# Optimization experiments

Hardware: AMD Instinct MI355X
Metric: run time of the kernel (lower is better)

Reference implementation:

```python
import jax, jax.numpy as jnp
import numpy as np

N, C, H, W, D = 4, 320, 16, 16, 16
POS_RATIO = 0.5


def setup_inputs() -> dict:
    key = jax.random.key(0)
    k1, k2, k3, k4 = jax.random.split(key, 4)
    q = jax.random.normal(k1, (N, C, H, W, D), jnp.float32)
    k = jax.random.normal(k2, (N, C, H, W, D), jnp.float32)

    def make_coord(kr):
        # crop boxes: upper-left corner in [0, 0.4), extent in [0.4, 0.6)
        start = jax.random.uniform(kr, (N, 3), jnp.float32) * 0.4
        size = 0.4 + jax.random.uniform(jax.random.fold_in(kr, 1), (N, 3), jnp.float32) * 0.2
        return jnp.concatenate([start, start + size], axis=1)  # (N, 6)

    coord_q = make_coord(k3)
    coord_k = make_coord(k4)
    return {"q": q, "k": k, "coord_q": coord_q, "coord_k": coord_k}


def _centers(coord, h, w, d):
    """coord: (N,6) -> centers (N, h*w*d, 3) of each voxel in global coords, and bin diag (N,)."""
    dims = jnp.array([h, w, d], jnp.float32)
    bin_sz = (coord[:, 3:6] - coord[:, 0:3]) / dims  # (N,3) = (bin_h, bin_w, bin_d)
    ax = jnp.arange(h, dtype=jnp.float32) + 0.5
    ay = jnp.arange(w, dtype=jnp.float32) + 0.5
    az = jnp.arange(d, dtype=jnp.float32) + 0.5
    grid = jnp.stack(jnp.meshgrid(ax, ay, az, indexing="ij"), axis=-1)  # (h,w,d,3)
    grid = grid.reshape(1, h * w * d, 3)
    centers = grid * bin_sz[:, None, :] + coord[:, None, 0:3]  # (N, L, 3)
    diag = jnp.sqrt(jnp.sum(bin_sz ** 2, axis=-1))  # (N,)
    return centers, diag


def reference(q, k, coord_q, coord_k):
    n, c, h, w, d = q.shape
    L = h * w * d
    qf = q.reshape(n, c, L)
    kf = k.reshape(n, c, L)

    cq, diag_q = _centers(coord_q, h, w, d)  # (N,L,3), (N,)
    ck, diag_k = _centers(coord_k, h, w, d)
    max_diag = jnp.maximum(diag_q, diag_k)[:, None, None]  # (N,1,1)

    def masked_loss(q_flat, centers_q):
        # pairwise center distance (N, L, L) -- sum of three squared diffs, no (N,L,L,3) stack
        d2 = ((centers_q[:, :, None, 0] - ck[:, None, :, 0]) ** 2
              + (centers_q[:, :, None, 1] - ck[:, None, :, 1]) ** 2
              + (centers_q[:, :, None, 2] - ck[:, None, :, 2]) ** 2)
        dist = jnp.sqrt(d2) / max_diag
        mask = jax.lax.stop_gradient((dist < POS_RATIO).astype(jnp.float32))
        logit = jnp.einsum("ncl,ncm->nlm", q_flat, kf)  # bmm(q^T, k)
        return jnp.sum(logit * mask, axis=(-2, -1)) / (jnp.sum(mask, axis=(-2, -1)) + 1e-6)

    loss = masked_loss(qf, cq)
    # anatomy branch: flip(q) and flipped q-centers along batch dim 0 (as in source flip(x, dim=0))
    loss_rev = masked_loss(jnp.flip(qf, axis=0), jnp.flip(cq, axis=0))
    return -2.0 * jnp.mean(loss) - 2.0 * jnp.mean(loss_rev)
```

## Files before the change

kernel.cpp:

```cpp
#include <hip/hip_runtime.h>

#define LVOX   4096
#define NCH    320
#define NCOMBO 8
#define PCAP   65536

struct Geo {
    float qs0, qs1, qs2, qo0, qo1, qo2;
    float ks0, ks1, ks2, ko0, ko1, ko2;
    float ik0, ik1, ik2;
    float T;
};

__device__ __forceinline__ Geo make_geo(const float* __restrict__ cq,
                                        const float* __restrict__ ck,
                                        int n, int qb) {
    Geo g;
    const float* qc = cq + qb * 6;
    const float* qn = cq + n * 6;
    const float* kc = ck + n * 6;
    g.qs0 = (qc[3] - qc[0]) * (1.f / 16.f); g.qo0 = qc[0];
    g.qs1 = (qc[4] - qc[1]) * (1.f / 16.f); g.qo1 = qc[1];
    g.qs2 = (qc[5] - qc[2]) * (1.f / 16.f); g.qo2 = qc[2];
    g.ks0 = (kc[3] - kc[0]) * (1.f / 16.f); g.ko0 = kc[0];
    g.ks1 = (kc[4] - kc[1]) * (1.f / 16.f); g.ko1 = kc[1];
    g.ks2 = (kc[5] - kc[2]) * (1.f / 16.f); g.ko2 = kc[2];
    g.ik0 = 1.f / g.ks0; g.ik1 = 1.f / g.ks1; g.ik2 = 1.f / g.ks2;
    float b0 = (qn[3] - qn[0]) * (1.f / 16.f);
    float b1 = (qn[4] - qn[1]) * (1.f / 16.f);
    float b2 = (qn[5] - qn[2]) * (1.f / 16.f);
    float dq = sqrtf(b0 * b0 + b1 * b1 + b2 * b2);
    float dk = sqrtf(g.ks0 * g.ks0 + g.ks1 * g.ks1 + g.ks2 * g.ks2);
    g.T = 0.5f * fmaxf(dq, dk);
    return g;
}

__device__ __forceinline__ void axrange(float c, float ko, float ik, float T,
                                        int& m0, int& m1) {
    float lo = (c - T - ko) * ik - 0.5f;
    float hi = (c + T - ko) * ik - 0.5f;
    m0 = max((int)ceilf(lo) - 1, 0);
    m1 = min((int)floorf(hi) + 1, 15);
}

__global__ void enum_pairs(const float* __restrict__ coord_q,
                           const float* __restrict__ coord_k,
                           unsigned* __restrict__ pcnt,
                           unsigned* __restrict__ pairs, int cap) {
    int gid = blockIdx.x * 256 + threadIdx.x;
    int j = gid >> 12;
    int l = gid & 4095;
    int n = j & 3;
    int qb = (j & 4) ? (3 - n) : n;
    Geo g = make_geo(coord_q, coord_k, n, qb);

    int ix = l >> 8, iy = (l >> 4) & 15, iz = l & 15;
    float cx = (ix + 0.5f) * g.qs0 + g.qo0;
    float cy = (iy + 0.5f) * g.qs1 + g.qo1;
    float cz = (iz + 0.5f) * g.qs2 + g.qo2;
    int x0, x1, y0, y1, z0, z1;
    axrange(cx, g.ko0, g.ik0, g.T, x0, x1);
    axrange(cy, g.ko1, g.ik1, g.T, y0, y1);
    axrange(cz, g.ko2, g.ik2, g.T, z0, z1);

    int nh = 0;
    for (int x = x0; x <= x1; ++x) {
        float dx = cx - ((x + 0.5f) * g.ks0 + g.ko0);
        float dx2 = dx * dx;
        for (int y = y0; y <= y1; ++y) {
            float dy = cy - ((y + 0.5f) * g.ks1 + g.ko1);
            float dxy = dx2 + dy * dy;
            for (int z = z0; z <= z1; ++z) {
                float dz = cz - ((z + 0.5f) * g.ks2 + g.ko2);
                if (sqrtf(dxy + dz * dz) < g.T) nh++;
            }
        }
    }

    int lane = threadIdx.x & 63;
    int incl = nh;
#pragma unroll
    for (int off = 1; off < 64; off <<= 1) {
        int t = __shfl_up(incl, off, 64);
        if (lane >= off) incl += t;
    }
    int total = __shfl(incl, 63, 64);
    int base = 0;
    if (lane == 63) base = (int)atomicAdd(&pcnt[j], (unsigned)total);
    base = __shfl(base, 63, 64);
    int w = base + incl - nh;

    unsigned* out = pairs + (size_t)j * (size_t)cap;
    for (int x = x0; x <= x1; ++x) {
        float dx = cx - ((x + 0.5f) * g.ks0 + g.ko0);
        float dx2 = dx * dx;
        for (int y = y0; y <= y1; ++y) {
            float dy = cy - ((y + 0.5f) * g.ks1 + g.ko1);
            float dxy = dx2 + dy * dy;
            for (int z = z0; z <= z1; ++z) {
                float dz = cz - ((z + 0.5f) * g.ks2 + g.ko2);
                if (sqrtf(dxy + dz * dz) < g.T) {
                    if (w < cap)
                        out[w] = ((unsigned)l << 12) | (unsigned)((x << 8) | (y << 4) | z);
                    w++;
                }
            }
        }
    }
}

__global__ void __launch_bounds__(256) gather_lds(
        const float* __restrict__ q, const float* __restrict__ k,
        const unsigned* __restrict__ pcnt, const unsigned* __restrict__ pairs,
        int cap, float* __restrict__ S) {
    __shared__ float qrow[LVOX];
    __shared__ float krow[LVOX];
    __shared__ float sp[4];
    int j = blockIdx.x;
    int c = blockIdx.y;
    int n = j & 3;
    int qb = (j & 4) ? (3 - n) : n;
    const float* qsrc = q + ((size_t)(qb * NCH + c)) * LVOX;
    const float* ksrc = k + ((size_t)(n * NCH + c)) * LVOX;
    int t = threadIdx.x;

#pragma unroll
    for (int i = 0; i < 4; ++i) {
        int off = (t + 256 * i) * 4;
        *(float4*)&qrow[off] = *(const float4*)&qsrc[off];
        *(float4*)&krow[off] = *(const float4*)&ksrc[off];
    }
    __syncthreads();

    unsigned cnt = pcnt[j];
    if (cnt > (unsigned)cap) cnt = (unsigned)cap;
    const unsigned* pl = pairs + (size_t)j * (size_t)cap;

    float acc = 0.f;
    for (unsigned p = (unsigned)t; p < cnt; p += 256u) {
        unsigned pr = pl[p];
        acc += qrow[pr >> 12] * krow[pr & 4095u];
    }

#pragma unroll
    for (int off = 32; off; off >>= 1) acc += __shfl_down(acc, off, 64);
    int lane = t & 63;
    if (lane == 0) sp[t >> 6] = acc;
    __syncthreads();
    if (t == 0) atomicAdd(&S[j], sp[0] + sp[1] + sp[2] + sp[3]);
}

__global__ void finalize(const float* __restrict__ S,
                         const unsigned* __restrict__ pcnt,
                         float* __restrict__ out) {
    if (threadIdx.x == 0) {
        float t = 0.f;
#pragma unroll
        for (int j = 0; j < NCOMBO; ++j)
            t += S[j] / ((float)pcnt[j] + 1e-6f);
        out[0] = -0.5f * t;
    }
}

extern "C" void kernel_launch(void* const* d_in, const int* in_sizes, int n_in,
                              void* d_out, int out_size, void* d_ws, size_t ws_size,
                              hipStream_t stream) {
    const float* q       = (const float*)d_in[0];
    const float* k       = (const float*)d_in[1];
    const float* coord_q = (const float*)d_in[2];
    const float* coord_k = (const float*)d_in[3];
    float* out = (float*)d_out;

    float*    S     = (float*)d_ws;
    unsigned* pcnt  = (unsigned*)d_ws + 8;
    unsigned* pairs = (unsigned*)d_ws + 16;

    size_t avail = (ws_size > 64) ? (ws_size / 4 - 16) / NCOMBO : 1;
    int cap = (int)((avail < (size_t)PCAP) ? avail : (size_t)PCAP);
    if (cap < 1) cap = 1;

    hipMemsetAsync(d_ws, 0, 64, stream);
    enum_pairs<<<(NCOMBO * LVOX) / 256, 256, 0, stream>>>(coord_q, coord_k, pcnt, pairs, cap);
    gather_lds<<<dim3(NCOMBO, NCH), 256, 0, stream>>>(q, k, pcnt, pairs, cap, S);
    finalize<<<1, 64, 0, stream>>>(S, pcnt, out);
}
```

Baseline: 144.1 us.

## Encode neighbor pairs as contiguous z-runs and gather sums per run

```diff
diff --git a/kernel.cpp b/kernel.cpp
--- a/kernel.cpp
+++ b/kernel.cpp
@@ -3,7 +3,7 @@
 #define LVOX   4096
 #define NCH    320
 #define NCOMBO 8
-#define PCAP   65536
+#define RCAP   49152
 
 struct Geo {
     float qs0, qs1, qs2, qo0, qo1, qo2;
@@ -43,10 +43,11 @@
     m1 = min((int)floorf(hi) + 1, 15);
 }
 
-__global__ void enum_pairs(const float* __restrict__ coord_q,
-                           const float* __restrict__ coord_k,
-                           unsigned* __restrict__ pcnt,
-                           unsigned* __restrict__ pairs, int cap) {
+__global__ void enum_runs(const float* __restrict__ coord_q,
+                          const float* __restrict__ coord_k,
+                          unsigned* __restrict__ pcnt,
+                          unsigned* __restrict__ rcnt,
+                          unsigned* __restrict__ runs, int cap) {
     int gid = blockIdx.x * 256 + threadIdx.x;
     int j = gid >> 12;
     int l = gid & 4095;
@@ -63,22 +64,24 @@
     axrange(cy, g.ko1, g.ik1, g.T, y0, y1);
     axrange(cz, g.ko2, g.ik2, g.T, z0, z1);
 
-    int nh = 0;
+    int nh = 0, nr = 0;
     for (int x = x0; x <= x1; ++x) {
         float dx = cx - ((x + 0.5f) * g.ks0 + g.ko0);
         float dx2 = dx * dx;
         for (int y = y0; y <= y1; ++y) {
             float dy = cy - ((y + 0.5f) * g.ks1 + g.ko1);
             float dxy = dx2 + dy * dy;
+            int zc = 0;
             for (int z = z0; z <= z1; ++z) {
                 float dz = cz - ((z + 0.5f) * g.ks2 + g.ko2);
-                if (sqrtf(dxy + dz * dz) < g.T) nh++;
+                if (sqrtf(dxy + dz * dz) < g.T) zc++;
             }
+            if (zc) { nr++; nh += zc; }
         }
     }
 
     int lane = threadIdx.x & 63;
-    int incl = nh;
+    int incl = nr;
 #pragma unroll
     for (int off = 1; off < 64; off <<= 1) {
         int t = __shfl_up(incl, off, 64);
@@ -86,36 +89,45 @@
     }
     int total = __shfl(incl, 63, 64);
     int base = 0;
-    if (lane == 63) base = (int)atomicAdd(&pcnt[j], (unsigned)total);
+    if (lane == 63) base = (int)atomicAdd(&rcnt[j], (unsigned)total);
     base = __shfl(base, 63, 64);
-    int w = base + incl - nh;
-
-    unsigned* out = pairs + (size_t)j * (size_t)cap;
+    int w = base + incl - nr;
+
+    int hsum = nh;
+#pragma unroll
+    for (int off = 32; off; off >>= 1) hsum += __shfl_down(hsum, off, 64);
+    if (lane == 0) atomicAdd(&pcnt[j], (unsigned)hsum);
+
+    unsigned* out = runs + (size_t)j * (size_t)cap;
     for (int x = x0; x <= x1; ++x) {
         float dx = cx - ((x + 0.5f) * g.ks0 + g.ko0);
         float dx2 = dx * dx;
         for (int y = y0; y <= y1; ++y) {
             float dy = cy - ((y + 0.5f) * g.ks1 + g.ko1);
             float dxy = dx2 + dy * dy;
+            int zf = -1, zc = 0;
             for (int z = z0; z <= z1; ++z) {
                 float dz = cz - ((z + 0.5f) * g.ks2 + g.ko2);
-                if (sqrtf(dxy + dz * dz) < g.T) {
-                    if (w < cap)
-                        out[w] = ((unsigned)l << 12) | (unsigned)((x << 8) | (y << 4) | z);
-                    w++;
-                }
+                if (sqrtf(dxy + dz * dz) < g.T) { if (!zc) zf = z; zc++; }
+            }
+            if (zc) {
+                if (w < cap)
+                    out[w] = ((unsigned)l << 16)
+                           | ((unsigned)((x << 8) | (y << 4) | zf) << 4)
+                           | (unsigned)(zc - 1);
+                w++;
             }
         }
     }
 }
 
-__global__ void __launch_bounds__(256) gather_lds(
+__global__ void __launch_bounds__(512) gather_runs(
         const float* __restrict__ q, const float* __restrict__ k,
-        const unsigned* __restrict__ pcnt, const unsigned* __restrict__ pairs,
+        const unsigned* __restrict__ rcnt, const unsigned* __restrict__ runs,
         int cap, float* __restrict__ S) {
     __shared__ float qrow[LVOX];
-    __shared__ float krow[LVOX];
-    __shared__ float sp[4];
+    __shared__ float krow[LVOX + 16];
+    __shared__ float sp[8];
     int j = blockIdx.x;
     int c = blockIdx.y;
     int n = j & 3;
@@ -125,21 +137,33 @@
     int t = threadIdx.x;
 
 #pragma unroll
-    for (int i = 0; i < 4; ++i) {
-        int off = (t + 256 * i) * 4;
+    for (int i = 0; i < 2; ++i) {
+        int off = (t + 512 * i) * 4;
         *(float4*)&qrow[off] = *(const float4*)&qsrc[off];
         *(float4*)&krow[off] = *(const float4*)&ksrc[off];
     }
+    if (t < 4) krow[LVOX + 4 * t] = 0.f;
     __syncthreads();
 
-    unsigned cnt = pcnt[j];
+    unsigned cnt = rcnt[j];
     if (cnt > (unsigned)cap) cnt = (unsigned)cap;
-    const unsigned* pl = pairs + (size_t)j * (size_t)cap;
+    const unsigned* rl = runs + (size_t)j * (size_t)cap;
 
     float acc = 0.f;
-    for (unsigned p = (unsigned)t; p < cnt; p += 256u) {
-        unsigned pr = pl[p];
-        acc += qrow[pr >> 12] * krow[pr & 4095u];
+    for (unsigned p = (unsigned)t * 4u; p < cnt; p += 512u * 4u) {
+        uint4 r4 = *(const uint4*)&rl[p];
+        unsigned rr[4] = {r4.x, r4.y, r4.z, r4.w};
+#pragma unroll
+        for (int e = 0; e < 4; ++e) {
+            bool valid = (p + (unsigned)e) < cnt;
+            unsigned pr = rr[e];
+            int l  = (int)(pr >> 16) & 4095;
+            int mb = (int)(pr >> 4) & 4095;
+            int len = (int)(pr & 15u) + 1;
+            float s = 0.f;
+            for (int i = 0; i < len; ++i) s += krow[mb + i];
+            acc += valid ? (qrow[l] * s) : 0.f;
+        }
     }
 
 #pragma unroll
@@ -147,7 +171,12 @@
     int lane = t & 63;
     if (lane == 0) sp[t >> 6] = acc;
     __syncthreads();
-    if (t == 0) atomicAdd(&S[j], sp[0] + sp[1] + sp[2] + sp[3]);
+    if (t == 0) {
+        float v = 0.f;
+#pragma unroll
+        for (int i = 0; i < 8; ++i) v += sp[i];
+        atomicAdd(&S[j], v);
+    }
 }
 
 __global__ void finalize(const float* __restrict__ S,
@@ -171,16 +200,18 @@
     const float* coord_k = (const float*)d_in[3];
     float* out = (float*)d_out;
 
-    float*    S     = (float*)d_ws;
-    unsigned* pcnt  = (unsigned*)d_ws + 8;
-    unsigned* pairs = (unsigned*)d_ws + 16;
-
-    size_t avail = (ws_size > 64) ? (ws_size / 4 - 16) / NCOMBO : 1;
-    int cap = (int)((avail < (size_t)PCAP) ? avail : (size_t)PCAP);
-    if (cap < 1) cap = 1;
-
-    hipMemsetAsync(d_ws, 0, 64, stream);
-    enum_pairs<<<(NCOMBO * LVOX) / 256, 256, 0, stream>>>(coord_q, coord_k, pcnt, pairs, cap);
-    gather_lds<<<dim3(NCOMBO, NCH), 256, 0, stream>>>(q, k, pcnt, pairs, cap, S);
+    float*    S    = (float*)d_ws;
+    unsigned* pcnt = (unsigned*)d_ws + 8;
+    unsigned* rcnt = (unsigned*)d_ws + 16;
+    unsigned* runs = (unsigned*)((char*)d_ws + 128);
+
+    size_t avail = (ws_size > 128) ? ((ws_size - 128) / 4) / NCOMBO : 4;
+    avail &= ~(size_t)3;
+    int cap = (int)((avail < (size_t)RCAP) ? avail : (size_t)RCAP);
+    if (cap < 4) cap = 4;
+
+    hipMemsetAsync(d_ws, 0, 128, stream);
+    enum_runs<<<(NCOMBO * LVOX) / 256, 256, 0, stream>>>(coord_q, coord_k, pcnt, rcnt, runs, cap);
+    gather_runs<<<dim3(NCOMBO, NCH), 512, 0, stream>>>(q, k, rcnt, runs, cap, S);
     finalize<<<1, 64, 0, stream>>>(S, pcnt, out);
 }
```

Result: faster. 139.1 us (-3.5%).
